# Optimization experiments

Measured on AMD Instinct MI355X. Metric: run time of the kernel, lower is better.

## Reference

```python
import jax, jax.numpy as jnp
import numpy as np

NEG_INF = -1e30

def setup_inputs() -> dict:
    key = jax.random.key(0)
    k1, k2, k3, k4, k5 = jax.random.split(key, 5)
    B, S, D, A = 16, 1024, 1024, 256
    hidden = jax.random.normal(k1, (B, S, D), dtype=jnp.float32)
    W1 = jax.random.normal(k2, (D, A), dtype=jnp.float32) / np.sqrt(D)
    b1 = jax.random.normal(k3, (A,), dtype=jnp.float32) * 0.01
    v = jax.random.normal(k4, (A,), dtype=jnp.float32) / np.sqrt(A)
    prompt_type_ids = jax.random.randint(k5, (B,), 0, 3, dtype=jnp.int32)
    return {"hidden": hidden, "W1": W1, "b1": b1, "v": v,
            "prompt_type_ids": prompt_type_ids}

def reference(hidden, W1, b1, v, prompt_type_ids):
    # hidden: [B,S,D]; per-token variable-length context attention pooling.
    B, S, D = hidden.shape
    # scores depend only on the context token l, not on the query position j
    attn_in = jnp.tanh(jnp.einsum('bsd,da->bsa', hidden, W1) + b1)  # [B,S,A]
    scores = jnp.einsum('bsa,a->bs', attn_in, v)                    # [B,S]

    idx = jnp.arange(S)
    j = idx[:, None]   # query position
    l = idx[None, :]   # context position
    prefix_m = l <= j          # h[:j+1]
    postfix_m = l >= j         # h[j:]
    cloze_m = l != j           # leave-one-out
    pt = prompt_type_ids[:, None, None]                              # [B,1,1]
    mask = jnp.where(pt == 0, prefix_m[None],
                     jnp.where(pt == 1, postfix_m[None], cloze_m[None]))  # [B,S,S] bool

    masked_scores = jnp.where(mask, scores[:, None, :], NEG_INF)    # [B,S(j),S(l)]
    p = jax.nn.softmax(masked_scores, axis=-1)                      # softmax over context
    cnt = jnp.sum(mask, axis=-1).astype(hidden.dtype)               # context length L per (b,j)
    # output = (1/L) * sum_l p_l * h_l  (the original's mean of p_l*h_l rows)
    pooled = jnp.einsum('bjl,bld->bjd', p, hidden) / cnt[..., None]
    return pooled
```

## Files before the change

### kernel.cpp

```cpp
#include <hip/hip_runtime.h>
#include <hip/hip_bf16.h>
#include <math.h>

#define SS 1024
#define DD 1024
#define AA 256
#define BB 16

typedef short short8 __attribute__((ext_vector_type(8)));
typedef float f32x4 __attribute__((ext_vector_type(4)));

static __device__ __forceinline__ short f2bf(float f) {
    __hip_bfloat16 h = __float2bfloat16(f);
    union { __hip_bfloat16 h; short s; } u; u.h = h;
    return u.s;
}

__global__ __launch_bounds__(256) void w1cvt_kernel(
    const float* __restrict__ W1, short* __restrict__ W1f)
{
    const int g  = blockIdx.x * 256 + threadIdx.x;
    const int l  = g & 63;
    const int nb = (g >> 6) & 15;
    const int kb = g >> 10;
    const int k0 = kb * 32 + ((l >> 4) << 3);
    const int n  = nb * 16 + (l & 15);
    short8 o;
    #pragma unroll
    for (int j = 0; j < 8; ++j) o[j] = f2bf(W1[(size_t)(k0 + j) * AA + n]);
    *reinterpret_cast<short8*>(&W1f[(size_t)g * 8]) = o;
}

__global__ __launch_bounds__(256) void scores_mfma_kernel(
    const float* __restrict__ hidden, const short* __restrict__ W1f,
    const float* __restrict__ b1, const float* __restrict__ v,
    float* __restrict__ scores)
{
    __shared__ float red[4][16];

    const int tid = threadIdx.x;
    const int w   = tid >> 6;
    const int l   = tid & 63;
    const int row0 = blockIdx.x * 16;

    const float*  ap = hidden + (size_t)(row0 + (l & 15)) * DD + ((l >> 4) << 3);
    const short8* bp = reinterpret_cast<const short8*>(W1f) + (size_t)(w * 4) * 64 + l;

    f32x4 acc[4];
    #pragma unroll
    for (int nb = 0; nb < 4; ++nb)
        #pragma unroll
        for (int r = 0; r < 4; ++r) acc[nb][r] = 0.f;

    #pragma unroll 2
    for (int kb = 0; kb < 32; ++kb) {
        const float4 av0 = *reinterpret_cast<const float4*>(ap + kb * 32);
        const float4 av1 = *reinterpret_cast<const float4*>(ap + kb * 32 + 4);
        short8 a;
        a[0] = f2bf(av0.x); a[1] = f2bf(av0.y); a[2] = f2bf(av0.z); a[3] = f2bf(av0.w);
        a[4] = f2bf(av1.x); a[5] = f2bf(av1.y); a[6] = f2bf(av1.z); a[7] = f2bf(av1.w);
        const short8* bkp = bp + (size_t)kb * 16 * 64;
        #pragma unroll
        for (int nb = 0; nb < 4; ++nb)
            acc[nb] = __builtin_amdgcn_mfma_f32_16x16x32_bf16(a, bkp[nb * 64], acc[nb], 0, 0, 0);
    }

    float b1l[4], vl[4];
    #pragma unroll
    for (int nb = 0; nb < 4; ++nb) {
        const int col = w * 64 + nb * 16 + (l & 15);
        b1l[nb] = b1[col];
        vl[nb]  = v[col];
    }
    #pragma unroll
    for (int r = 0; r < 4; ++r) {
        float s = tanhf(acc[0][r] + b1l[0]) * vl[0]
                + tanhf(acc[1][r] + b1l[1]) * vl[1]
                + tanhf(acc[2][r] + b1l[2]) * vl[2]
                + tanhf(acc[3][r] + b1l[3]) * vl[3];
        s += __shfl_xor(s, 1, 64);
        s += __shfl_xor(s, 2, 64);
        s += __shfl_xor(s, 4, 64);
        s += __shfl_xor(s, 8, 64);
        if ((l & 15) == 0) red[w][((l >> 4) << 2) + r] = s;
    }
    __syncthreads();
    if (tid < 16)
        scores[row0 + tid] = red[0][tid] + red[1][tid] + red[2][tid] + red[3][tid];
}

__global__ __launch_bounds__(1024) void pool_kernel(
    const float* __restrict__ hidden, const float* __restrict__ scores,
    const int* __restrict__ pt, float* __restrict__ out)
{
    __shared__ float e_s[1024];
    __shared__ float iv_s[1024];
    __shared__ float seg[16][64];
    __shared__ float wmax[16];
    __shared__ float wsum[16];

    const int tid  = threadIdx.x;
    const int wave = tid >> 6;
    const int lane = tid & 63;
    const int b    = blockIdx.x >> 4;
    const int d    = (blockIdx.x & 15) * 64 + lane;

    const float s = scores[b * SS + tid];
    float mx = s;
    #pragma unroll
    for (int off = 32; off > 0; off >>= 1) mx = fmaxf(mx, __shfl_xor(mx, off, 64));
    if (lane == 0) wmax[wave] = mx;
    __syncthreads();
    float m = wmax[0];
    #pragma unroll
    for (int i = 1; i < 16; ++i) m = fmaxf(m, wmax[i]);

    const float e = expf(s - m);
    float ps = e;
    #pragma unroll
    for (int off = 1; off < 64; off <<= 1) {
        const float t = __shfl_up(ps, off, 64);
        if (lane >= off) ps += t;
    }
    if (lane == 63) wsum[wave] = ps;
    __syncthreads();
    float pre = 0.f, Z = 0.f;
    #pragma unroll
    for (int i = 0; i < 16; ++i) {
        const float t = wsum[i];
        if (i < wave) pre += t;
        Z += t;
    }
    const float P = ps + pre;

    const int type = pt[b];
    float iv;
    if (type == 0)        iv = 1.f / (P * (float)(tid + 1));
    else if (type == 1)   iv = 1.f / ((Z - P + e) * (float)(SS - tid));
    else                  iv = 1.f / ((Z - e) * (float)(SS - 1));
    e_s[tid]  = e;
    iv_s[tid] = iv;
    __syncthreads();

    const float* hb = hidden + (size_t)b * SS * DD + d;
    float*       ob = out    + (size_t)b * SS * DD + d;
    const int l0 = wave * 64;

    float a0 = 0.f, a1 = 0.f, a2 = 0.f, a3 = 0.f;
    #pragma unroll
    for (int i = 0; i < 64; i += 4) {
        const int j = l0 + i;
        a0 += e_s[j + 0] * hb[(size_t)(j + 0) * DD];
        a1 += e_s[j + 1] * hb[(size_t)(j + 1) * DD];
        a2 += e_s[j + 2] * hb[(size_t)(j + 2) * DD];
        a3 += e_s[j + 3] * hb[(size_t)(j + 3) * DD];
    }
    seg[wave][lane] = (a0 + a1) + (a2 + a3);
    __syncthreads();

    if (type == 0) {
        float run = 0.f;
        for (int w2 = 0; w2 < wave; ++w2) run += seg[w2][lane];
        #pragma unroll 4
        for (int i = 0; i < 64; ++i) {
            const int j = l0 + i;
            run += e_s[j] * hb[(size_t)j * DD];
            __builtin_nontemporal_store(run * iv_s[j], &ob[(size_t)j * DD]);
        }
    } else if (type == 1) {
        float run = 0.f;
        for (int w2 = wave + 1; w2 < 16; ++w2) run += seg[w2][lane];
        #pragma unroll 4
        for (int i = 63; i >= 0; --i) {
            const int j = l0 + i;
            run += e_s[j] * hb[(size_t)j * DD];
            __builtin_nontemporal_store(run * iv_s[j], &ob[(size_t)j * DD]);
        }
    } else {
        float T = 0.f;
        #pragma unroll
        for (int w2 = 0; w2 < 16; ++w2) T += seg[w2][lane];
        #pragma unroll 4
        for (int i = 0; i < 64; ++i) {
            const int j = l0 + i;
            __builtin_nontemporal_store((T - e_s[j] * hb[(size_t)j * DD]) * iv_s[j],
                                        &ob[(size_t)j * DD]);
        }
    }
}

extern "C" void kernel_launch(void* const* d_in, const int* in_sizes, int n_in,
                              void* d_out, int out_size, void* d_ws, size_t ws_size,
                              hipStream_t stream) {
    const float* hidden = (const float*)d_in[0];
    const float* W1     = (const float*)d_in[1];
    const float* b1     = (const float*)d_in[2];
    const float* v      = (const float*)d_in[3];
    const int*   pt     = (const int*)  d_in[4];
    float* out = (float*)d_out;

    float* ws     = (float*)d_ws;
    float* scores = ws;
    short* W1f    = (short*)(ws + BB * SS);

    w1cvt_kernel      <<<128, 256, 0, stream>>>(W1, W1f);
    scores_mfma_kernel<<<(BB * SS) / 16, 256, 0, stream>>>(hidden, W1f, b1, v, scores);
    pool_kernel       <<<BB * (DD / 64), 1024, 0, stream>>>(hidden, scores, pt, out);
}
```

Before: 179.7 us.

## Stage W1 tiles in LDS with double buffering and cache hidden in pool registers

The scores GEMM now has each block handle 32 rows instead of 16. Each W1 bf16 tile is loaded once per block into LDS through global_load_lds, with double buffering and prefetching of the next hidden fragment, so B-operand reuse doubles and load latency overlaps the MFMAs. The pool kernel loads its 64 hidden values per lane into registers once instead of reading global memory twice, and fully unrolls the store loops. The trade-off is higher register pressure (64 floats per thread at 1024 threads) and 64KB of LDS per scores block, which may reduce occupancy.

New measurement: 252.6 us. 1.41x slower.

```diff
diff --git a/kernel.cpp b/kernel.cpp
--- a/kernel.cpp
+++ b/kernel.cpp
@@ -9,6 +9,9 @@
 
 typedef short short8 __attribute__((ext_vector_type(8)));
 typedef float f32x4 __attribute__((ext_vector_type(4)));
+
+typedef __attribute__((address_space(1))) const void gconst_t;
+typedef __attribute__((address_space(3))) void lds_t;
 
 static __device__ __forceinline__ short f2bf(float f) {
     __hip_bfloat16 h = __float2bfloat16(f);
@@ -36,33 +39,94 @@
     const float* __restrict__ b1, const float* __restrict__ v,
     float* __restrict__ scores)
 {
-    __shared__ float red[4][16];
-
-    const int tid = threadIdx.x;
-    const int w   = tid >> 6;
-    const int l   = tid & 63;
-    const int row0 = blockIdx.x * 16;
-
-    const float*  ap = hidden + (size_t)(row0 + (l & 15)) * DD + ((l >> 4) << 3);
-    const short8* bp = reinterpret_cast<const short8*>(W1f) + (size_t)(w * 4) * 64 + l;
-
-    f32x4 acc[4];
-    #pragma unroll
-    for (int nb = 0; nb < 4; ++nb)
-        #pragma unroll
-        for (int r = 0; r < 4; ++r) acc[nb][r] = 0.f;
-
-    #pragma unroll 2
-    for (int kb = 0; kb < 32; ++kb) {
-        const float4 av0 = *reinterpret_cast<const float4*>(ap + kb * 32);
-        const float4 av1 = *reinterpret_cast<const float4*>(ap + kb * 32 + 4);
-        short8 a;
-        a[0] = f2bf(av0.x); a[1] = f2bf(av0.y); a[2] = f2bf(av0.z); a[3] = f2bf(av0.w);
-        a[4] = f2bf(av1.x); a[5] = f2bf(av1.y); a[6] = f2bf(av1.z); a[7] = f2bf(av1.w);
-        const short8* bkp = bp + (size_t)kb * 16 * 64;
+    __shared__ short Bl[2][16384];
+    __shared__ float red[4][32];
+
+    const int tid  = threadIdx.x;
+    const int w    = tid >> 6;
+    const int l    = tid & 63;
+    const int row0 = blockIdx.x * 32;
+
+    const float* ha = hidden + (size_t)(row0 + (l & 15)) * DD + ((l >> 4) << 3);
+    const short* wsrc = W1f + w * 512 + l * 8;
+
+    f32x4 acc[2][4];
+    #pragma unroll
+    for (int mi = 0; mi < 2; ++mi)
         #pragma unroll
         for (int nb = 0; nb < 4; ++nb)
-            acc[nb] = __builtin_amdgcn_mfma_f32_16x16x32_bf16(a, bkp[nb * 64], acc[nb], 0, 0, 0);
+            #pragma unroll
+            for (int r = 0; r < 4; ++r) acc[mi][nb][r] = 0.f;
+
+    float4 pf[2][2][2];
+
+    #pragma unroll
+    for (int q = 0; q < 8; ++q)
+        __builtin_amdgcn_global_load_lds(
+            (gconst_t*)(wsrc + (size_t)q * 2048),
+            (lds_t*)(&Bl[0][w * 512 + q * 2048]), 16, 0, 0);
+    #pragma unroll
+    for (int mi = 0; mi < 2; ++mi)
+        #pragma unroll
+        for (int kbl = 0; kbl < 2; ++kbl)
+            #pragma unroll
+            for (int h = 0; h < 2; ++h)
+                pf[mi][kbl][h] = *reinterpret_cast<const float4*>(
+                    ha + (size_t)(mi * 16) * DD + kbl * 32 + h * 4);
+    asm volatile("s_waitcnt vmcnt(0)" ::: "memory");
+    __builtin_amdgcn_s_barrier();
+    __builtin_amdgcn_sched_barrier(0);
+
+    int cur = 0;
+    for (int t = 0; t < 16; ++t) {
+        short8 a[2][2];
+        #pragma unroll
+        for (int mi = 0; mi < 2; ++mi)
+            #pragma unroll
+            for (int kbl = 0; kbl < 2; ++kbl) {
+                a[mi][kbl][0] = f2bf(pf[mi][kbl][0].x);
+                a[mi][kbl][1] = f2bf(pf[mi][kbl][0].y);
+                a[mi][kbl][2] = f2bf(pf[mi][kbl][0].z);
+                a[mi][kbl][3] = f2bf(pf[mi][kbl][0].w);
+                a[mi][kbl][4] = f2bf(pf[mi][kbl][1].x);
+                a[mi][kbl][5] = f2bf(pf[mi][kbl][1].y);
+                a[mi][kbl][6] = f2bf(pf[mi][kbl][1].z);
+                a[mi][kbl][7] = f2bf(pf[mi][kbl][1].w);
+            }
+
+        if (t < 15) {
+            const short* ws = wsrc + (size_t)(t + 1) * 16384;
+            #pragma unroll
+            for (int q = 0; q < 8; ++q)
+                __builtin_amdgcn_global_load_lds(
+                    (gconst_t*)(ws + (size_t)q * 2048),
+                    (lds_t*)(&Bl[cur ^ 1][w * 512 + q * 2048]), 16, 0, 0);
+            #pragma unroll
+            for (int mi = 0; mi < 2; ++mi)
+                #pragma unroll
+                for (int kbl = 0; kbl < 2; ++kbl)
+                    #pragma unroll
+                    for (int h = 0; h < 2; ++h)
+                        pf[mi][kbl][h] = *reinterpret_cast<const float4*>(
+                            ha + (size_t)(mi * 16) * DD + (t + 1) * 64 + kbl * 32 + h * 4);
+        }
+
+        #pragma unroll
+        for (int kbl = 0; kbl < 2; ++kbl)
+            #pragma unroll
+            for (int nb = 0; nb < 4; ++nb) {
+                const short8 bf = *reinterpret_cast<const short8*>(
+                    &Bl[cur][(kbl * 16 + w * 4 + nb) * 512 + l * 8]);
+                acc[0][nb] = __builtin_amdgcn_mfma_f32_16x16x32_bf16(a[0][kbl], bf, acc[0][nb], 0, 0, 0);
+                acc[1][nb] = __builtin_amdgcn_mfma_f32_16x16x32_bf16(a[1][kbl], bf, acc[1][nb], 0, 0, 0);
+            }
+
+        if (t < 15) {
+            asm volatile("s_waitcnt vmcnt(0)" ::: "memory");
+            __builtin_amdgcn_s_barrier();
+            __builtin_amdgcn_sched_barrier(0);
+        }
+        cur ^= 1;
     }
 
     float b1l[4], vl[4];
@@ -73,19 +137,22 @@
         vl[nb]  = v[col];
     }
     #pragma unroll
-    for (int r = 0; r < 4; ++r) {
-        float s = tanhf(acc[0][r] + b1l[0]) * vl[0]
-                + tanhf(acc[1][r] + b1l[1]) * vl[1]
-                + tanhf(acc[2][r] + b1l[2]) * vl[2]
-                + tanhf(acc[3][r] + b1l[3]) * vl[3];
-        s += __shfl_xor(s, 1, 64);
-        s += __shfl_xor(s, 2, 64);
-        s += __shfl_xor(s, 4, 64);
-        s += __shfl_xor(s, 8, 64);
-        if ((l & 15) == 0) red[w][((l >> 4) << 2) + r] = s;
-    }
-    __syncthreads();
-    if (tid < 16)
+    for (int mi = 0; mi < 2; ++mi) {
+        #pragma unroll
+        for (int r = 0; r < 4; ++r) {
+            float s = tanhf(acc[mi][0][r] + b1l[0]) * vl[0]
+                    + tanhf(acc[mi][1][r] + b1l[1]) * vl[1]
+                    + tanhf(acc[mi][2][r] + b1l[2]) * vl[2]
+                    + tanhf(acc[mi][3][r] + b1l[3]) * vl[3];
+            s += __shfl_xor(s, 1, 64);
+            s += __shfl_xor(s, 2, 64);
+            s += __shfl_xor(s, 4, 64);
+            s += __shfl_xor(s, 8, 64);
+            if ((l & 15) == 0) red[w][mi * 16 + ((l >> 4) << 2) + r] = s;
+        }
+    }
+    __syncthreads();
+    if (tid < 32)
         scores[row0 + tid] = red[0][tid] + red[1][tid] + red[2][tid] + red[3][tid];
 }
 
@@ -146,14 +213,17 @@
     float*       ob = out    + (size_t)b * SS * DD + d;
     const int l0 = wave * 64;
 
+    float hv[64];
+    #pragma unroll
+    for (int i = 0; i < 64; ++i) hv[i] = hb[(size_t)(l0 + i) * DD];
+
     float a0 = 0.f, a1 = 0.f, a2 = 0.f, a3 = 0.f;
     #pragma unroll
     for (int i = 0; i < 64; i += 4) {
-        const int j = l0 + i;
-        a0 += e_s[j + 0] * hb[(size_t)(j + 0) * DD];
-        a1 += e_s[j + 1] * hb[(size_t)(j + 1) * DD];
-        a2 += e_s[j + 2] * hb[(size_t)(j + 2) * DD];
-        a3 += e_s[j + 3] * hb[(size_t)(j + 3) * DD];
+        a0 += e_s[l0 + i + 0] * hv[i + 0];
+        a1 += e_s[l0 + i + 1] * hv[i + 1];
+        a2 += e_s[l0 + i + 2] * hv[i + 2];
+        a3 += e_s[l0 + i + 3] * hv[i + 3];
     }
     seg[wave][lane] = (a0 + a1) + (a2 + a3);
     __syncthreads();
@@ -161,29 +231,29 @@
     if (type == 0) {
         float run = 0.f;
         for (int w2 = 0; w2 < wave; ++w2) run += seg[w2][lane];
-        #pragma unroll 4
+        #pragma unroll
         for (int i = 0; i < 64; ++i) {
             const int j = l0 + i;
-            run += e_s[j] * hb[(size_t)j * DD];
+            run += e_s[j] * hv[i];
             __builtin_nontemporal_store(run * iv_s[j], &ob[(size_t)j * DD]);
         }
     } else if (type == 1) {
         float run = 0.f;
         for (int w2 = wave + 1; w2 < 16; ++w2) run += seg[w2][lane];
-        #pragma unroll 4
+        #pragma unroll
         for (int i = 63; i >= 0; --i) {
             const int j = l0 + i;
-            run += e_s[j] * hb[(size_t)j * DD];
+            run += e_s[j] * hv[i];
             __builtin_nontemporal_store(run * iv_s[j], &ob[(size_t)j * DD]);
         }
     } else {
         float T = 0.f;
         #pragma unroll
         for (int w2 = 0; w2 < 16; ++w2) T += seg[w2][lane];
-        #pragma unroll 4
+        #pragma unroll
         for (int i = 0; i < 64; ++i) {
             const int j = l0 + i;
-            __builtin_nontemporal_store((T - e_s[j] * hb[(size_t)j * DD]) * iv_s[j],
+            __builtin_nontemporal_store((T - e_s[j] * hv[i]) * iv_s[j],
                                         &ob[(size_t)j * DD]);
         }
     }
@@ -204,6 +274,6 @@
     short* W1f    = (short*)(ws + BB * SS);
 
     w1cvt_kernel      <<<128, 256, 0, stream>>>(W1, W1f);
-    scores_mfma_kernel<<<(BB * SS) / 16, 256, 0, stream>>>(hidden, W1f, b1, v, scores);
+    scores_mfma_kernel<<<(BB * SS) / 32, 256, 0, stream>>>(hidden, W1f, b1, v, scores);
     pool_kernel       <<<BB * (DD / 64), 1024, 0, stream>>>(hidden, scores, pt, out);
 }
```
